# Kernel optimization log

Measured on AMD Instinct MI355X. Metric: run time of the kernel, lower is better.

The kernel has to match this reference:

```python
import jax, jax.numpy as jnp
import numpy as np
from jax import lax

B, EMB, CIN, COUT, K, H, W = 16, 768, 64, 64, 3, 112, 112
HID = EMB // 4  # reduction_ratio=4
TOTAL = COUT * CIN * K * K


def setup_inputs() -> dict:
    key = jax.random.key(0)
    k1, k2, k3, k4 = jax.random.split(key, 4)
    cls_token = jax.random.normal(k1, (B, 1, EMB), dtype=jnp.float32)
    features = jax.random.normal(k2, (B, CIN, H, W), dtype=jnp.float32)
    W1 = jax.random.normal(k3, (EMB, HID), dtype=jnp.float32) * 0.02
    b1 = jnp.zeros((HID,), dtype=jnp.float32)
    W2 = jax.random.normal(k4, (HID, TOTAL), dtype=jnp.float32) * 0.01
    b2 = jnp.zeros((TOTAL,), dtype=jnp.float32)
    return {"cls_token": cls_token, "features": features,
            "W1": W1, "b1": b1, "W2": W2, "b2": b2}


def _per_sample_conv(feat, kern):
    # feat: (CIN, H, W); kern: (COUT, CIN, K, K) -> (COUT, H, W)
    out = lax.conv_general_dilated(
        feat[None], kern, window_strides=(1, 1), padding="SAME",
        dimension_numbers=("NCHW", "OIHW", "NCHW"))
    return out[0]


def reference(cls_token, features, W1, b1, W2, b2):
    # Dynamic kernel generation from CLS token
    x = cls_token[:, 0, :]                      # (B, EMB)
    h = jax.nn.relu(x @ W1 + b1)                # (B, HID)
    params = jnp.tanh(h @ W2 + b2)              # (B, TOTAL)
    kernel = params.reshape(B, COUT, CIN, K, K)
    # Per-sample convolution (equivalent to unfold + bmm in torch)
    conv_feat = jax.vmap(_per_sample_conv)(features, kernel)  # (B, COUT, H, W)
    # in_channels == out_channels -> identity shortcut
    return conv_feat + features
```

## Files before the change

kernel.cpp:

```cpp
#include <hip/hip_runtime.h>
#include <hip/hip_bf16.h>

#define BB   16
#define EMB  768
#define CIN  64
#define COUT 64
#define HH   112
#define WW   112
#define HID  192
#define TOTAL 36864
#define KSZ  576
#define PW   114
#define CELL 128
#define ROWB (PW * CELL)

typedef short bf16x8 __attribute__((ext_vector_type(8)));
typedef float f32x4  __attribute__((ext_vector_type(4)));
typedef int   i32x4  __attribute__((ext_vector_type(4)));

static __device__ __forceinline__ unsigned short f2bf(float f) {
    unsigned u = __float_as_uint(f);
    u += 0x7FFF + ((u >> 16) & 1);
    return (unsigned short)(u >> 16);
}

static __device__ __forceinline__ bf16x8 pack8(const float* v) {
    bf16x8 r;
    #pragma unroll
    for (int j = 0; j < 8; ++j) r[j] = (short)f2bf(v[j]);
    return r;
}

#define GLOAD_LDS16(g, l) \
    __builtin_amdgcn_global_load_lds((const __attribute__((address_space(1))) void*)(g), \
                                     (__attribute__((address_space(3))) void*)(l), 16, 0, 0)

__global__ __launch_bounds__(256) void mlp1_kernel(const float* __restrict__ cls,
                                                   const float* __restrict__ W1,
                                                   const float* __restrict__ b1,
                                                   float* __restrict__ h) {
    __shared__ float xs[EMB];
    __shared__ float red[16][17];
    const int b   = blockIdx.x / 12;
    const int jg  = blockIdx.x - 12 * b;
    const int tid = threadIdx.x;
    for (int i = tid; i < EMB; i += 256) xs[i] = cls[b * EMB + i];
    __syncthreads();
    const int j16 = tid & 15;
    const int kq  = tid >> 4;
    const int j   = jg * 16 + j16;
    float acc = 0.f;
    #pragma unroll
    for (int k = kq * 48; k < kq * 48 + 48; ++k) acc += xs[k] * W1[k * HID + j];
    red[j16][kq] = acc;
    __syncthreads();
    if (tid < 16) {
        float s = b1[jg * 16 + tid];
        #pragma unroll
        for (int q = 0; q < 16; ++q) s += red[tid][q];
        h[b * HID + jg * 16 + tid] = fmaxf(s, 0.f);
    }
}

__global__ __launch_bounds__(256) void pre_mlp2(const float* __restrict__ feat,
                                                unsigned short* __restrict__ P,
                                                const float* __restrict__ h,
                                                const float* __restrict__ W2,
                                                const float* __restrict__ b2,
                                                unsigned short* __restrict__ Ag) {
    __shared__ float hs[16 * 193];
    const int bid = blockIdx.x;
    const int tid = threadIdx.x;

    if (bid < HH * BB) {
        const int j = bid >> 3;
        const int b = (bid & 7) * 2 + (j >= 112 ? 1 : 0);
        const int y = j - (j >= 112 ? 112 : 0);
        unsigned short* Prow = P + ((size_t)b * PW + y + 1) * (PW * 64);
        if (tid < 16) {
            const int cell = (tid >> 3) ? (PW - 1) : 0;
            *(i32x4*)((char*)Prow + cell * CELL + (tid & 7) * 16) = (i32x4){0, 0, 0, 0};
        }
        const int o = tid >> 5;
        const int q = tid & 31;
        if (q < 28) {
            const float* fb = feat + (((size_t)b * CIN + o * 8) * HH + y) * WW + 4 * q;
            f32x4 v[8];
            #pragma unroll
            for (int j2 = 0; j2 < 8; ++j2) v[j2] = *(const f32x4*)(fb + (size_t)j2 * (HH * WW));
            #pragma unroll
            for (int i = 0; i < 4; ++i) {
                unsigned short w[8];
                #pragma unroll
                for (int j2 = 0; j2 < 8; ++j2) w[j2] = f2bf(v[j2][i]);
                *(bf16x8*)(Prow + (size_t)(4 * q + i + 1) * 64 + o * 8) = *(bf16x8*)w;
            }
        }
    } else if (bid < HH * BB + 32) {
        const int idx = bid - HH * BB;
        const int b   = idx & 15;
        unsigned short* Prow = P + ((size_t)b * PW + ((idx >> 4) ? (PW - 1) : 0)) * (PW * 64);
        #pragma unroll
        for (int k = 0; k < 4; ++k) {
            const int i = tid + 256 * k;
            if (i < 912) ((i32x4*)Prow)[i] = (i32x4){0, 0, 0, 0};
        }
    } else {
        const int blk = bid - (HH * BB + 32);
        for (int i = tid; i < BB * HID; i += 256) {
            const int bb = i / HID;
            hs[bb * 193 + (i - bb * HID)] = h[i];
        }
        __syncthreads();
        const int wave = tid >> 6;
        const int lane = tid & 63;
        const int lg   = lane >> 4;
        const int ln   = lane & 15;
        const int t0   = (blk * 4 + wave) * 16;

        bf16x8 a6[6];
        #pragma unroll
        for (int kk = 0; kk < 6; ++kk) {
            float v[8];
            #pragma unroll
            for (int j = 0; j < 8; ++j) v[j] = hs[ln * 193 + kk * 32 + lg * 8 + j];
            a6[kk] = pack8(v);
        }

        f32x4 acc = (f32x4){0.f, 0.f, 0.f, 0.f};
        #pragma unroll
        for (int kk = 0; kk < 6; ++kk) {
            float w[8];
            #pragma unroll
            for (int j = 0; j < 8; ++j)
                w[j] = W2[(size_t)(kk * 32 + lg * 8 + j) * TOTAL + t0 + ln];
            acc = __builtin_amdgcn_mfma_f32_16x16x32_bf16(a6[kk], pack8(w), acc, 0, 0, 0);
        }

        const int t    = t0 + ln;
        const float bias = b2[t];
        const int co  = t / KSZ;
        const int rem = t - co * KSZ;
        const int ci  = rem / 9;
        const int p9  = rem - ci * 9;
        const float idv = (p9 == 4 && co == ci) ? 1.f : 0.f;
        unsigned short* pA = Ag + (size_t)(p9 * 64 + co) * 64 + ci;
        #pragma unroll
        for (int rg = 0; rg < 4; ++rg) {
            const int bi = lg * 4 + rg;
            pA[(size_t)bi * TOTAL] = f2bf(tanhf(acc[rg] + bias) + idv);
        }
    }
}

__global__ __launch_bounds__(128, 2) void conv_kernel(const unsigned short* __restrict__ Ag,
                                                      const unsigned short* __restrict__ P,
                                                      float* __restrict__ out) {
    __shared__ __align__(16) char lds[4 * ROWB];
    const int tid = threadIdx.x;
    const int bid   = (blockIdx.x & 7) * 112 + (blockIdx.x >> 3);
    const int b     = bid / 56;
    const int strip = bid - b * 56;
    const int y0    = strip * 2;

    const int r    = tid >> 6;
    const int lane = tid & 63;
    const int lg   = lane >> 4;
    const int ln   = lane & 15;

    const char* Pb = (const char*)P + ((size_t)b * PW + y0) * ROWB;
    #pragma unroll
    for (int k = 0; k < 28; ++k) {
        const int i = k * 128 + tid;
        const int s = i / 912;
        const int jj = i - s * 912;
        const int c = jj >> 3, g = jj & 7;
        GLOAD_LDS16(Pb + (size_t)s * ROWB + c * CELL + ((g ^ (c & 7)) << 4),
                    lds + (size_t)i * 16);
    }
    if (tid < 64) {
        const int i = 3584 + tid;
        const int jj = i - 3 * 912;
        const int c = jj >> 3, g = jj & 7;
        GLOAD_LDS16(Pb + (size_t)3 * ROWB + c * CELL + ((g ^ (c & 7)) << 4),
                    lds + (size_t)i * 16);
    }

    const unsigned short* Ab = Ag + (size_t)b * 9 * 4096;

    f32x4 acc[4][7];
    #pragma unroll
    for (int ct = 0; ct < 4; ++ct)
        #pragma unroll
        for (int t = 0; t < 7; ++t) acc[ct][t] = (f32x4){0.f, 0.f, 0.f, 0.f};

    asm volatile("s_waitcnt vmcnt(0)" ::: "memory");
    __builtin_amdgcn_s_barrier();
    __builtin_amdgcn_sched_barrier(0);

    #pragma unroll
    for (int cib = 0; cib < 2; ++cib) {
        #pragma unroll
        for (int p9 = 0; p9 < 9; ++p9) {
            const int kh = p9 / 3, kw = p9 - 3 * kh;
            bf16x8 af[4];
            #pragma unroll
            for (int ct = 0; ct < 4; ++ct)
                af[ct] = *(const bf16x8*)(Ab + (size_t)(p9 * 64 + ct * 16 + ln) * 64
                                          + cib * 32 + lg * 8);
            const char* lbase = lds + (r + kh) * ROWB + (ln + kw) * CELL;
            const int   sw    = (((cib * 4 + lg) ^ ((ln + kw) & 7)) << 4);
            #pragma unroll
            for (int t = 0; t < 7; ++t) {
                const bf16x8 bf = *(const bf16x8*)(lbase + t * (16 * CELL) + sw);
                #pragma unroll
                for (int ct = 0; ct < 4; ++ct)
                    acc[ct][t] = __builtin_amdgcn_mfma_f32_16x16x32_bf16(af[ct], bf, acc[ct][t], 0, 0, 0);
            }
        }
    }

    const int y = y0 + r;
    float* ob = out + (((size_t)b * COUT + lg * 4) * HH + y) * WW + ln;
    #pragma unroll
    for (int ct = 0; ct < 4; ++ct)
        #pragma unroll
        for (int t = 0; t < 7; ++t)
            #pragma unroll
            for (int rg = 0; rg < 4; ++rg)
                ob[((size_t)(ct * 16 + rg)) * HH * WW + t * 16] = acc[ct][t][rg];
}

extern "C" void kernel_launch(void* const* d_in, const int* in_sizes, int n_in,
                              void* d_out, int out_size, void* d_ws, size_t ws_size,
                              hipStream_t stream) {
    const float* cls      = (const float*)d_in[0];
    const float* features = (const float*)d_in[1];
    const float* W1       = (const float*)d_in[2];
    const float* b1       = (const float*)d_in[3];
    const float* W2       = (const float*)d_in[4];
    const float* b2       = (const float*)d_in[5];
    float* out = (float*)d_out;

    float*          h  = (float*)d_ws;
    unsigned short* Ag = (unsigned short*)(h + BB * HID);
    unsigned short* P  = Ag + (size_t)BB * 9 * 4096;

    mlp1_kernel<<<192, 256, 0, stream>>>(cls, W1, b1, h);
    pre_mlp2<<<HH * BB + 32 + 576, 256, 0, stream>>>(features, P, h, W2, b2, Ag);
    conv_kernel<<<896, 128, 0, stream>>>(Ag, P, out);
}
```

Baseline: 62.90 us.

## Drop LDS staging in conv kernel, read padded input directly from global; add nontemporal hints

The conv kernel no longer stages the 4 padded input rows into LDS with global_load_lds and a barrier. Each wave now reads its B fragments straight from global memory (through the cache), and the loop order is swapped so p9 is outer and cib inner. Nontemporal hints are added to the feature loads, the W2 loads and the output stores. This removes the LDS fill latency and the barrier, and frees LDS so more blocks can be resident. In exchange, neighbouring kernel taps now reload overlapping data from L1/L2 instead of LDS, which raises global traffic and exposes load latency directly in front of the MFMAs.

Result: slower. 90.37 us (+43.7%).

```diff
diff --git a/kernel.cpp b/kernel.cpp
--- a/kernel.cpp
+++ b/kernel.cpp
@@ -30,10 +30,6 @@
     for (int j = 0; j < 8; ++j) r[j] = (short)f2bf(v[j]);
     return r;
 }
-
-#define GLOAD_LDS16(g, l) \
-    __builtin_amdgcn_global_load_lds((const __attribute__((address_space(1))) void*)(g), \
-                                     (__attribute__((address_space(3))) void*)(l), 16, 0, 0)
 
 __global__ __launch_bounds__(256) void mlp1_kernel(const float* __restrict__ cls,
                                                    const float* __restrict__ W1,
@@ -87,7 +83,8 @@
             const float* fb = feat + (((size_t)b * CIN + o * 8) * HH + y) * WW + 4 * q;
             f32x4 v[8];
             #pragma unroll
-            for (int j2 = 0; j2 < 8; ++j2) v[j2] = *(const f32x4*)(fb + (size_t)j2 * (HH * WW));
+            for (int j2 = 0; j2 < 8; ++j2)
+                v[j2] = __builtin_nontemporal_load((const f32x4*)(fb + (size_t)j2 * (HH * WW)));
             #pragma unroll
             for (int i = 0; i < 4; ++i) {
                 unsigned short w[8];
@@ -133,7 +130,7 @@
             float w[8];
             #pragma unroll
             for (int j = 0; j < 8; ++j)
-                w[j] = W2[(size_t)(kk * 32 + lg * 8 + j) * TOTAL + t0 + ln];
+                w[j] = __builtin_nontemporal_load(W2 + (size_t)(kk * 32 + lg * 8 + j) * TOTAL + t0 + ln);
             acc = __builtin_amdgcn_mfma_f32_16x16x32_bf16(a6[kk], pack8(w), acc, 0, 0, 0);
         }
 
@@ -156,7 +153,6 @@
 __global__ __launch_bounds__(128, 2) void conv_kernel(const unsigned short* __restrict__ Ag,
                                                       const unsigned short* __restrict__ P,
                                                       float* __restrict__ out) {
-    __shared__ __align__(16) char lds[4 * ROWB];
     const int tid = threadIdx.x;
     const int bid   = (blockIdx.x & 7) * 112 + (blockIdx.x >> 3);
     const int b     = bid / 56;
@@ -168,25 +164,8 @@
     const int lg   = lane >> 4;
     const int ln   = lane & 15;
 
-    const char* Pb = (const char*)P + ((size_t)b * PW + y0) * ROWB;
-    #pragma unroll
-    for (int k = 0; k < 28; ++k) {
-        const int i = k * 128 + tid;
-        const int s = i / 912;
-        const int jj = i - s * 912;
-        const int c = jj >> 3, g = jj & 7;
-        GLOAD_LDS16(Pb + (size_t)s * ROWB + c * CELL + ((g ^ (c & 7)) << 4),
-                    lds + (size_t)i * 16);
-    }
-    if (tid < 64) {
-        const int i = 3584 + tid;
-        const int jj = i - 3 * 912;
-        const int c = jj >> 3, g = jj & 7;
-        GLOAD_LDS16(Pb + (size_t)3 * ROWB + c * CELL + ((g ^ (c & 7)) << 4),
-                    lds + (size_t)i * 16);
-    }
-
     const unsigned short* Ab = Ag + (size_t)b * 9 * 4096;
+    const char* Pb = (const char*)P + ((size_t)b * PW + y0 + r) * ROWB;
 
     f32x4 acc[4][7];
     #pragma unroll
@@ -194,29 +173,26 @@
         #pragma unroll
         for (int t = 0; t < 7; ++t) acc[ct][t] = (f32x4){0.f, 0.f, 0.f, 0.f};
 
-    asm volatile("s_waitcnt vmcnt(0)" ::: "memory");
-    __builtin_amdgcn_s_barrier();
-    __builtin_amdgcn_sched_barrier(0);
-
-    #pragma unroll
-    for (int cib = 0; cib < 2; ++cib) {
-        #pragma unroll
-        for (int p9 = 0; p9 < 9; ++p9) {
-            const int kh = p9 / 3, kw = p9 - 3 * kh;
+    #pragma unroll
+    for (int p9 = 0; p9 < 9; ++p9) {
+        const int kh = p9 / 3, kw = p9 - 3 * kh;
+        const char* prow = Pb + kh * ROWB + (ln + kw) * CELL;
+        #pragma unroll
+        for (int cib = 0; cib < 2; ++cib) {
             bf16x8 af[4];
             #pragma unroll
             for (int ct = 0; ct < 4; ++ct)
                 af[ct] = *(const bf16x8*)(Ab + (size_t)(p9 * 64 + ct * 16 + ln) * 64
                                           + cib * 32 + lg * 8);
-            const char* lbase = lds + (r + kh) * ROWB + (ln + kw) * CELL;
-            const int   sw    = (((cib * 4 + lg) ^ ((ln + kw) & 7)) << 4);
-            #pragma unroll
-            for (int t = 0; t < 7; ++t) {
-                const bf16x8 bf = *(const bf16x8*)(lbase + t * (16 * CELL) + sw);
+            bf16x8 bf[7];
+            #pragma unroll
+            for (int t = 0; t < 7; ++t)
+                bf[t] = *(const bf16x8*)(prow + t * (16 * CELL) + cib * 64 + lg * 16);
+            #pragma unroll
+            for (int t = 0; t < 7; ++t)
                 #pragma unroll
                 for (int ct = 0; ct < 4; ++ct)
-                    acc[ct][t] = __builtin_amdgcn_mfma_f32_16x16x32_bf16(af[ct], bf, acc[ct][t], 0, 0, 0);
-            }
+                    acc[ct][t] = __builtin_amdgcn_mfma_f32_16x16x32_bf16(af[ct], bf[t], acc[ct][t], 0, 0, 0);
         }
     }
 
@@ -228,7 +204,8 @@
         for (int t = 0; t < 7; ++t)
             #pragma unroll
             for (int rg = 0; rg < 4; ++rg)
-                ob[((size_t)(ct * 16 + rg)) * HH * WW + t * 16] = acc[ct][t][rg];
+                __builtin_nontemporal_store(acc[ct][t][rg],
+                                            ob + ((size_t)(ct * 16 + rg)) * HH * WW + t * 16);
 }
 
 extern "C" void kernel_launch(void* const* d_in, const int* in_sizes, int n_in,
```
